# Performance work log

Measured on AMD Instinct MI355X. Metric: run time of the kernel, lower is better.

## Reference

```python
import jax, jax.numpy as jnp
import numpy as np

B, D, H, L, E, NL, P, IMG, NT = 32, 768, 8, 6, 8, 256, 16, 224, 10
G = IMG // P          # 14 patches per side
NP = G * G            # 196 patches
HD = D // H           # 96 head dim
TOPK = 2
KEEP = 0.25
EPS = 1e-5


def layer_norm(x, g, b):
    m = x.mean(-1, keepdims=True)
    v = ((x - m) ** 2).mean(-1, keepdims=True)
    return (x - m) / jnp.sqrt(v + EPS) * g + b


def mha(q, kv, in_w, in_b, out_w, out_b):
    # torch nn.MultiheadAttention: packed in_proj (3D, D), out_proj (D, D)
    wq, wk, wv = in_w[:D], in_w[D:2 * D], in_w[2 * D:]
    bq, bk, bv = in_b[:D], in_b[D:2 * D], in_b[2 * D:]

    def heads(x, w, b):
        y = x @ w.T + b                               # (B, S, D)
        return y.reshape(x.shape[0], x.shape[1], H, HD).transpose(0, 2, 1, 3)

    Q = heads(q, wq, bq)
    K = heads(kv, wk, bk)
    V = heads(kv, wv, bv)
    scores = jnp.einsum('bhqd,bhkd->bhqk', Q, K) / np.sqrt(HD).astype(np.float32)
    attn = jax.nn.softmax(scores, axis=-1)
    o = jnp.einsum('bhqk,bhkd->bhqd', attn, V)
    o = o.transpose(0, 2, 1, 3).reshape(q.shape[0], q.shape[1], D)
    return o @ out_w.T + out_b


def moe(x, rw, rb, w1, b1, w2, b2):
    # top-2 routing; renormalize the top-k weights with a second softmax
    Bq, S, _ = x.shape
    T = Bq * S
    xt = x.reshape(T, D)
    probs = jax.nn.softmax(xt @ rw.T + rb, axis=-1)       # (T, E)
    tw, ti = jax.lax.top_k(probs, TOPK)                   # (T, K)
    tw = jax.nn.softmax(tw, axis=-1)
    # combine weights per expert: (T, E), >0 only for the chosen experts
    combine = (jax.nn.one_hot(ti, E, dtype=x.dtype) * tw[..., None]).sum(axis=1)
    out = jnp.zeros_like(xt)
    for e in range(E):  # fixed small expert count
        h = jax.nn.gelu(xt @ w1[e].T + b1[e], approximate=False)
        out = out + (h @ w2[e].T + b2[e]) * combine[:, e:e + 1]
    return out.reshape(Bq, S, D)


def _forward(images, type_ids, mask_noise, conv_w, conv_b, pos_emb, type_emb,
             latents, ca_in_w, ca_in_b, ca_out_w, ca_out_b, ca_ln_g, ca_ln_b,
             sa_in_w, sa_in_b, sa_out_w, sa_out_b, ln1_g, ln1_b,
             router_w, router_b, e_w1, e_b1, e_w2, e_b2, ln2_g, ln2_b):
    b = images.shape[0]
    # non-overlapping conv patch embed == unfold + matmul
    xp = images.reshape(b, 3, G, P, G, P).transpose(0, 2, 4, 1, 3, 5)
    xp = xp.reshape(b, NP, 3 * P * P)
    patches = xp @ conv_w.reshape(D, -1).T + conv_b        # (B, NP, D)
    patches = patches + pos_emb + type_emb[type_ids][:, None, :]
    # random masking: keep n_visible patches chosen by argsort of noise
    n_visible = int(NP * KEEP)
    order = jnp.argsort(mask_noise, axis=1)
    visible_indices = order[:, :n_visible]
    masked_indices = order[:, n_visible:]
    visible = jnp.take_along_axis(patches, visible_indices[:, :, None], axis=1)
    # cross attention from latents to visible patches
    lat = jnp.broadcast_to(latents, (b, NL, D))
    lat = layer_norm(lat + mha(lat, visible, ca_in_w, ca_in_b, ca_out_w, ca_out_b),
                     ca_ln_g, ca_ln_b)
    for l in range(L):
        a = mha(lat, lat, sa_in_w[l], sa_in_b[l], sa_out_w[l], sa_out_b[l])
        lat = layer_norm(lat + a, ln1_g[l], ln1_b[l])
        m = moe(lat, router_w[l], router_b[l], e_w1[l], e_b1[l], e_w2[l], e_b2[l])
        lat = layer_norm(lat + m, ln2_g[l], ln2_b[l])
    return lat, visible_indices, masked_indices


def setup_inputs() -> dict:
    key = jax.random.key(0)
    ks = jax.random.split(key, 16)
    r = lambda k, shape, s=0.02: jax.random.normal(k, shape, dtype=jnp.float32) * s
    z = lambda shape: jnp.zeros(shape, jnp.float32)
    o = lambda shape: jnp.ones(shape, jnp.float32)
    inp = {}
    inp['images'] = jax.random.normal(ks[0], (B, 3, IMG, IMG), dtype=jnp.float32)
    inp['type_ids'] = jax.random.randint(ks[1], (B,), 0, NT)
    inp['mask_noise'] = jax.random.uniform(ks[2], (B, NP), dtype=jnp.float32)
    inp['conv_w'] = r(ks[3], (D, 3, P, P))
    inp['conv_b'] = z((D,))
    inp['pos_emb'] = r(ks[4], (1, NP, D), 1.0)
    inp['type_emb'] = r(ks[5], (NT, D), 1.0)
    inp['latents'] = r(ks[6], (NL, D), 1.0)
    inp['ca_in_w'] = r(ks[7], (3 * D, D)); inp['ca_in_b'] = z((3 * D,))
    inp['ca_out_w'] = r(ks[8], (D, D)); inp['ca_out_b'] = z((D,))
    inp['ca_ln_g'] = o((D,)); inp['ca_ln_b'] = z((D,))
    inp['sa_in_w'] = r(ks[9], (L, 3 * D, D)); inp['sa_in_b'] = z((L, 3 * D))
    inp['sa_out_w'] = r(ks[10], (L, D, D)); inp['sa_out_b'] = z((L, D))
    inp['ln1_g'] = o((L, D)); inp['ln1_b'] = z((L, D))
    inp['router_w'] = r(ks[11], (L, E, D)); inp['router_b'] = z((L, E))
    inp['e_w1'] = r(ks[12], (L, E, 2 * D, D)); inp['e_b1'] = z((L, E, 2 * D))
    inp['e_w2'] = r(ks[13], (L, E, D, 2 * D)); inp['e_b2'] = z((L, E, D))
    inp['ln2_g'] = o((L, D)); inp['ln2_b'] = z((L, D))
    return inp


def reference(images, type_ids, mask_noise, conv_w, conv_b, pos_emb, type_emb,
              latents, ca_in_w, ca_in_b, ca_out_w, ca_out_b, ca_ln_g, ca_ln_b,
              sa_in_w, sa_in_b, sa_out_w, sa_out_b, ln1_g, ln1_b,
              router_w, router_b, e_w1, e_b1, e_w2, e_b2, ln2_g, ln2_b):
    return _forward(images, type_ids, mask_noise, conv_w, conv_b, pos_emb,
                    type_emb, latents, ca_in_w, ca_in_b, ca_out_w, ca_out_b,
                    ca_ln_g, ca_ln_b, sa_in_w, sa_in_b, sa_out_w, sa_out_b,
                    ln1_g, ln1_b, router_w, router_b, e_w1, e_b1, e_w2, e_b2,
                    ln2_g, ln2_b)
```

## Files before the change

kernel.cpp:

```cpp
#include <hip/hip_runtime.h>

typedef unsigned short u16;
typedef unsigned int u32;
typedef __attribute__((ext_vector_type(8))) u16 u16x8;
typedef __attribute__((ext_vector_type(8))) __bf16 bf16x8;
typedef __attribute__((ext_vector_type(4))) float f32x4;

#define DEV static __device__ __forceinline__

DEV float b2f(u16 u){ unsigned int i = ((unsigned int)u)<<16; float f; __builtin_memcpy(&f,&i,4); return f; }
DEV u16 f2b(float f){ unsigned int x; __builtin_memcpy(&x,&f,4); x = x + 0x7fffu + ((x>>16)&1u); return (u16)(x>>16); }

DEV void gll16(const u16* g, u16* l){
    __builtin_amdgcn_global_load_lds(
        (const __attribute__((address_space(1))) u32*)(const void*)g,
        (__attribute__((address_space(3))) u32*)(void*)l, 16, 0, 0);
}

template<bool F32>
DEV u16x8 ld8(const void* base, long off){
    if constexpr (F32){
        const float* p = (const float*)base + off;
        float4 a = *(const float4*)p;
        float4 b = *(const float4*)(p+4);
        u16x8 r;
        r[0]=f2b(a.x); r[1]=f2b(a.y); r[2]=f2b(a.z); r[3]=f2b(a.w);
        r[4]=f2b(b.x); r[5]=f2b(b.y); r[6]=f2b(b.z); r[7]=f2b(b.w);
        return r;
    } else {
        return *(const u16x8*)((const u16*)base + off);
    }
}
template<bool F32>
DEV const void* vadd(const void* p, long elems){
    if constexpr (F32) return (const void*)((const float*)p + elems);
    else               return (const void*)((const u16*)p + elems);
}

#define LAT_ELEMS 6291456
#define NVIS 49
#define NMASK 147
#define T_TOK 8192
#define MOE_CAP 17408
#define MOE_HALF 8704
#define KOFF 6291456L
#define VOFF 12582912L

__global__ __launch_bounds__(256) void wconv(const float* __restrict__ src, u16* __restrict__ dst, long n)
{
    long i = ((long)blockIdx.x*256 + threadIdx.x)*8;
    if (i >= n) return;
    *(u16x8*)(dst + i) = ld8<true>(src, i);
}

__global__ __launch_bounds__(256) void argsort_k(const float* __restrict__ noise,
                                                 int* __restrict__ order,
                                                 float* __restrict__ dout,
                                                 u16* __restrict__ zbuf)
{
    __shared__ float vals[196];
    __shared__ int ord[196];
    int b = blockIdx.x, tid = threadIdx.x;
    if (b == 0 && tid < 128) zbuf[tid] = 0;
    if (tid < 196) vals[tid] = noise[b*196 + tid];
    __syncthreads();
    if (tid < 196){
        float vi = vals[tid]; int rank = 0;
        for (int j=0;j<196;j++){ float vj = vals[j]; rank += (vj < vi) || (vj == vi && j < tid); }
        ord[rank] = tid;
    }
    __syncthreads();
    if (tid < 196){
        int v = ord[tid];
        order[b*196 + tid] = v;
        if (tid < NVIS) dout[LAT_ELEMS + b*NVIS + tid] = (float)v;
        else            dout[LAT_ELEMS + 32*NVIS + b*NMASK + (tid - NVIS)] = (float)v;
    }
}

__global__ __launch_bounds__(256) void patch_gather(const float* __restrict__ images,
                                                    const int* __restrict__ order,
                                                    u16* __restrict__ Ap)
{
    int i = blockIdx.x*256 + threadIdx.x;
    int t = i/48, kc = i - t*48;
    if (t >= 1664) return;
    if (t >= 1568){
        u16x8 z{};
        *(u16x8*)(Ap + (long)t*768 + kc*16)     = z;
        *(u16x8*)(Ap + (long)t*768 + kc*16 + 8) = z;
        return;
    }
    int b = t/49, vi = t - b*49;
    int p = order[b*196 + vi];
    int c = kc >> 4, py = kc & 15;
    int gy = p/14, gx = p - gy*14;
    const float* src = images + (((long)(b*3 + c)*224 + gy*16 + py)*224 + gx*16);
    u16x8 o0 = ld8<true>(src, 0);
    u16x8 o1 = ld8<true>(src, 8);
    *(u16x8*)(Ap + (long)t*768 + kc*16)     = o0;
    *(u16x8*)(Ap + (long)t*768 + kc*16 + 8) = o1;
}

__global__ __launch_bounds__(256) void add_pos_type(u16* __restrict__ vis,
                                                    const int* __restrict__ order,
                                                    const int* __restrict__ type_ids,
                                                    const float* __restrict__ pos,
                                                    const float* __restrict__ temb)
{
    int i = blockIdx.x*256 + threadIdx.x;
    int t = i/96, dc = (i - t*96)*8;
    if (t >= 1568) return;
    int b = t/49, vi = t - b*49;
    int p = order[b*196 + vi], tb = type_ids[b];
    u16x8 a = *(u16x8*)(vis + (long)t*768 + dc);
    const float* pp = pos  + (long)p*768 + dc;
    const float* tt = temb + (long)tb*768 + dc;
    float4 p0 = *(const float4*)pp, p1 = *(const float4*)(pp+4);
    float4 t0 = *(const float4*)tt, t1 = *(const float4*)(tt+4);
    u16x8 o;
    o[0]=f2b(b2f(a[0])+p0.x+t0.x); o[1]=f2b(b2f(a[1])+p0.y+t0.y);
    o[2]=f2b(b2f(a[2])+p0.z+t0.z); o[3]=f2b(b2f(a[3])+p0.w+t0.w);
    o[4]=f2b(b2f(a[4])+p1.x+t1.x); o[5]=f2b(b2f(a[5])+p1.y+t1.y);
    o[6]=f2b(b2f(a[6])+p1.z+t1.z); o[7]=f2b(b2f(a[7])+p1.w+t1.w);
    *(u16x8*)(vis + (long)t*768 + dc) = o;
}

template<int BK, int MT, bool BIAS, bool GELU, int GRP, bool AF32, bool BF32, bool SWZ, bool GLL>
__global__ __launch_bounds__(256,4) void gemm_nt(
    const void* __restrict__ A, const void* __restrict__ B, const float* __restrict__ bias,
    u16* __restrict__ C,
    int M, int N, int K, int lda, int ldb, int ldc,
    float scale, int ZLO, int NB,
    long sAh, long sAl, long sBh, long sBl, long sCh, long sCl,
    const int* __restrict__ aoff, const int* __restrict__ tos, const u16* __restrict__ zbuf,
    int row_base, long sBE, long sBiasE)
{
    int bx = blockIdx.x, by = blockIdx.y;
    if (SWZ){
        int nx = gridDim.x, ny = gridDim.y;
        int nwg = nx*ny;
        int flat = by*nx + bx;
        int q = nwg >> 3, r = nwg & 7;
        int xcd = flat & 7, idx = flat >> 3;
        int wg = (xcd < r ? xcd*(q+1) : r*(q+1) + (xcd - r)*q) + idx;
        bx = wg % nx; by = wg / nx;
    }
    int z = blockIdx.z; int zh = z / ZLO, zl = z - zh*ZLO;
    const void* Ab = vadd<AF32>(A, zh*sAh + zl*sAl);
    const void* Bb = vadd<BF32>(B, zh*sBh + zl*sBl);
    u16* Cb = C + zh*sCh + zl*sCl;
    const float* biasb = bias;
    int row0 = by*MT, col0 = bx*128;
    int lim = 0;
    if (GRP == 1 || GRP == 2){
        lim = aoff[8];
        int g0 = row_base + row0;
        if (g0 >= lim) return;
        int e = 0;
        #pragma unroll
        for (int i=1;i<8;i++) if (g0 >= aoff[i]) e = i;
        Bb = vadd<BF32>(B, (long)e*sBE);
        if (BIAS) biasb = bias + (long)e*sBiasE;
    }
    constexpr int SP = GLL ? BK : BK + 8;
    constexpr int MR = MT/32;
    __shared__ __align__(16) u16 As[MT*SP];
    __shared__ __align__(16) u16 Bs[128*SP];
    int tid = threadIdx.x;
    int lane = tid & 63, wv = tid >> 6;
    int wr = (wv>>1)*(MT/2), wc = (wv&1)*64;
    f32x4 acc[MR][4];
    #pragma unroll
    for (int m=0;m<MR;m++){
        #pragma unroll
        for (int n=0;n<4;n++) acc[m][n] = f32x4{0.f,0.f,0.f,0.f};
    }
    constexpr int RPC = BK/8;
    constexpr int RPI = 64/RPC;
    constexpr int NJA = MT*RPC/256;
    constexpr int NJB = 128*RPC/256;
    constexpr int PER = 128*RPC/256;
    int tA[4];
    if (GRP == 1){
        #pragma unroll
        for (int j=0;j<NJA;j++){
            int r = wv*(MT/4) + j*RPI + (lane/RPC);
            tA[j] = tos[row_base + row0 + r];
        }
    }
    for (int k0=0; k0<K; k0+=BK){
        if constexpr (GLL){
            int ch = lane % RPC;
            #pragma unroll
            for (int j=0;j<NJA;j++){
                int r  = wv*(MT/4) + j*RPI + (lane/RPC);
                const u16* sa;
                if (GRP == 1){
                    int t = tA[j];
                    sa = (t >= 0) ? (const u16*)Ab + (long)t*lda + k0 + ch*8 : zbuf + ch*8;
                } else {
                    sa = (const u16*)Ab + (long)(row0+r)*lda + k0 + ch*8;
                }
                gll16(sa, As + (wv*(MT/4) + j*RPI)*BK);
            }
            #pragma unroll
            for (int j=0;j<NJB;j++){
                int r = wv*32 + j*RPI + (lane/RPC);
                const u16* sb = (col0 + r < NB) ? (const u16*)Bb + (long)(col0+r)*ldb + k0 + ch*8
                                                : zbuf + ch*8;
                gll16(sb, Bs + (wv*32 + j*RPI)*BK);
            }
        } else if constexpr (MT == 128){
            #pragma unroll
            for (int j=0;j<PER;j++){
                int c = j*256 + tid;
                int r = c / RPC, cc = (c - r*RPC)*8;
                u16x8 va{}, vb{};
                if (GRP == 1){
                    int t = tA[j];
                    if (t >= 0) va = ld8<AF32>(Ab, (long)t*lda + k0 + cc);
                } else {
                    va = ld8<AF32>(Ab, (long)(row0+r)*lda + k0 + cc);
                }
                if (col0 + r < NB) vb = ld8<BF32>(Bb, (long)(col0+r)*ldb + k0 + cc);
                *(u16x8*)(As + r*SP + cc) = va;
                *(u16x8*)(Bs + r*SP + cc) = vb;
            }
        }
        __syncthreads();
        #pragma unroll
        for (int kk=0; kk<BK/32; kk++){
            bf16x8 af[MR], bg[4];
            #pragma unroll
            for (int m=0;m<MR;m++)
                af[m] = *(const bf16x8*)(As + (wr + m*16 + (lane&15))*SP + kk*32 + (lane>>4)*8);
            #pragma unroll
            for (int n=0;n<4;n++)
                bg[n] = *(const bf16x8*)(Bs + (wc + n*16 + (lane&15))*SP + kk*32 + (lane>>4)*8);
            #pragma unroll
            for (int m=0;m<MR;m++){
                #pragma unroll
                for (int n=0;n<4;n++)
                    acc[m][n] = __builtin_amdgcn_mfma_f32_16x16x32_bf16(af[m], bg[n], acc[m][n], 0,0,0);
            }
        }
        __syncthreads();
    }
    if (GRP == 3){
        #pragma unroll
        for (int m=0;m<MR;m++){
            int rbase = row0 + wr + m*16 + ((lane>>4)<<2);
            #pragma unroll
            for (int n=0;n<4;n++){
                int col = col0 + wc + n*16 + (lane&15);
                float bv = biasb[col];
                if (col < 1536){
                    u16* base = (col < 768) ? Cb : Cb + sBE - 768;
                    #pragma unroll
                    for (int j=0;j<4;j++)
                        base[(long)(rbase+j)*768 + col] = f2b(acc[m][n][j]*scale + bv);
                } else {
                    int c96 = col - 1536;
                    int h = c96/96, d = c96 - h*96;
                    ushort4 o4;
                    o4.x = f2b(acc[m][n][0]*scale + bv);
                    o4.y = f2b(acc[m][n][1]*scale + bv);
                    o4.z = f2b(acc[m][n][2]*scale + bv);
                    o4.w = f2b(acc[m][n][3]*scale + bv);
                    *(ushort4*)(Cb + sBiasE + ((long)((rbase>>8)*8 + h)*96 + d)*256 + (rbase & 255)) = o4;
                }
            }
        }
        return;
    }
    #pragma unroll
    for (int m=0;m<MR;m++){
        int rbase = row0 + wr + m*16 + ((lane>>4)<<2);
        #pragma unroll
        for (int n=0;n<4;n++){
            int col = col0 + wc + n*16 + (lane&15);
            if (col < N){
                float bv = BIAS ? biasb[col] : 0.f;
                #pragma unroll
                for (int j=0;j<4;j++){
                    int row = rbase + j;
                    bool ok = (row < M);
                    if (GRP == 1 || GRP == 2) ok = ok && (row_base + row) < lim;
                    if (ok){
                        float v = acc[m][n][j]*scale + bv;
                        if (GELU) v = 0.5f*v*(1.f + erff(v*0.70710678118f));
                        u16 ov = f2b(v);
                        if (GRP == 2){
                            Cb[(long)(row_base + row)*ldc + col] = ov;
                        } else {
                            Cb[(long)row*ldc + col] = ov;
                        }
                    }
                }
            }
        }
    }
}

__global__ __launch_bounds__(256,4) void scores_sm(const u16* __restrict__ Q,
                                                   const u16* __restrict__ K,
                                                   u16* __restrict__ S)
{
    __shared__ __align__(16) u16 As[64*32];
    __shared__ __align__(16) u16 Bs[256*32];
    int z = blockIdx.y;
    int b = z >> 3, h = z & 7;
    const u16* Ab = Q + (long)b*196608 + h*96 + (long)blockIdx.x*64*768;
    const u16* Bb = K + (long)b*196608 + h*96;
    int tid = threadIdx.x, lane = tid & 63, wv = tid >> 6;
    f32x4 acc[16];
    #pragma unroll
    for (int n=0;n<16;n++) acc[n] = f32x4{0.f,0.f,0.f,0.f};
    int ch = lane & 3, rr = lane >> 2;
    for (int k0=0;k0<96;k0+=32){
        gll16(Ab + (long)(wv*16 + rr)*768 + k0 + ch*8, As + (wv*16)*32);
        #pragma unroll
        for (int jj=0;jj<4;jj++)
            gll16(Bb + (long)(wv*64 + jj*16 + rr)*768 + k0 + ch*8, Bs + (wv*64 + jj*16)*32);
        __syncthreads();
        bf16x8 af = *(const bf16x8*)(As + (wv*16 + (lane&15))*32 + (lane>>4)*8);
        #pragma unroll
        for (int n=0;n<16;n++){
            bf16x8 bg = *(const bf16x8*)(Bs + (n*16 + (lane&15))*32 + (lane>>4)*8);
            acc[n] = __builtin_amdgcn_mfma_f32_16x16x32_bf16(af, bg, acc[n], 0,0,0);
        }
        __syncthreads();
    }
    const float SCL = 0.10206207f;
    u16* Sz = S + (long)z*65536 + (long)blockIdx.x*64*256;
    #pragma unroll
    for (int j=0;j<4;j++){
        float mx = -1e30f;
        #pragma unroll
        for (int n=0;n<16;n++) mx = fmaxf(mx, acc[n][j]);
        #pragma unroll
        for (int off=8; off>=1; off>>=1) mx = fmaxf(mx, __shfl_xor(mx, off, 64));
        float ev[16]; float sum = 0.f;
        #pragma unroll
        for (int n=0;n<16;n++){ ev[n] = __expf((acc[n][j]-mx)*SCL); sum += ev[n]; }
        #pragma unroll
        for (int off=8; off>=1; off>>=1) sum += __shfl_xor(sum, off, 64);
        float inv = 1.f/sum;
        int row = wv*16 + ((lane>>4)<<2) + j;
        #pragma unroll
        for (int n=0;n<16;n++) Sz[(long)row*256 + n*16 + (lane&15)] = f2b(ev[n]*inv);
    }
}

__global__ __launch_bounds__(256) void ca_attn(const u16* __restrict__ Qc,
                                               const u16* __restrict__ KV,
                                               u16* __restrict__ attn_out)
{
    __shared__ float Sm[256*49];
    __shared__ u16 KVs[49*96];
    int b = blockIdx.x, h = blockIdx.y, q = threadIdx.x;
    for (int i=q; i<49*96; i+=256){ int k=i/96, d=i-k*96; KVs[i] = KV[(long)(b*49+k)*1536 + h*96 + d]; }
    __syncthreads();
    float qv[96];
    #pragma unroll
    for (int d=0;d<96;d++) qv[d] = b2f(Qc[(long)q*768 + h*96 + d]);
    for (int k=0;k<49;k++){
        float a = 0.f;
        #pragma unroll
        for (int d=0;d<96;d++) a += qv[d]*b2f(KVs[k*96+d]);
        Sm[q*49+k] = a*0.10206207f;
    }
    __syncthreads();
    for (int i=q; i<49*96; i+=256){ int k=i/96, d=i-k*96; KVs[i] = KV[(long)(b*49+k)*1536 + 768 + h*96 + d]; }
    float mx = -1e30f;
    for (int k=0;k<49;k++) mx = fmaxf(mx, Sm[q*49+k]);
    float sum = 0.f;
    for (int k=0;k<49;k++){ float e = __expf(Sm[q*49+k]-mx); Sm[q*49+k]=e; sum+=e; }
    float inv = 1.f/sum;
    __syncthreads();
    for (int d=0;d<96;d++){
        float a = 0.f;
        for (int k=0;k<49;k++) a += Sm[q*49+k]*b2f(KVs[k*96+d]);
        attn_out[(long)(b*256+q)*768 + h*96 + d] = f2b(a*inv);
    }
}

template<int MODE, bool ROUTE>
__global__ __launch_bounds__(256) void ln_k(
    const float* __restrict__ res, int resmod,
    const u16* __restrict__ add,
    const u16* __restrict__ OutE, const int* __restrict__ sot, const float2* __restrict__ w01,
    const float* __restrict__ g, const float* __restrict__ bb,
    const float* __restrict__ rw, const float* __restrict__ rb,
    int2* __restrict__ e01o, float2* __restrict__ w01o,
    float* __restrict__ out, u16* __restrict__ outb, int T)
{
    int wid = threadIdx.x >> 6, lane = threadIdx.x & 63;
    int t = blockIdx.x*4 + wid; if (t >= T) return;
    const float* rp = res + (long)(t % resmod)*768;
    float x[12];
    #pragma unroll
    for (int j=0;j<3;j++){
        float4 v = *(const float4*)(rp + j*256 + lane*4);
        x[j*4+0]=v.x; x[j*4+1]=v.y; x[j*4+2]=v.z; x[j*4+3]=v.w;
    }
    if (MODE == 0){
        const u16* ap = add + (long)t*768;
        #pragma unroll
        for (int j=0;j<3;j++){
            ushort4 v = *(const ushort4*)(ap + j*256 + lane*4);
            x[j*4+0]+=b2f(v.x); x[j*4+1]+=b2f(v.y); x[j*4+2]+=b2f(v.z); x[j*4+3]+=b2f(v.w);
        }
    } else {
        int s0 = sot[2*t], s1 = sot[2*t+1];
        float2 w = w01[t];
        const u16* p0 = OutE + (long)s0*768;
        const u16* p1 = OutE + (long)s1*768;
        #pragma unroll
        for (int j=0;j<3;j++){
            ushort4 v0 = *(const ushort4*)(p0 + j*256 + lane*4);
            ushort4 v1 = *(const ushort4*)(p1 + j*256 + lane*4);
            x[j*4+0] += w.x*b2f(v0.x) + w.y*b2f(v1.x);
            x[j*4+1] += w.x*b2f(v0.y) + w.y*b2f(v1.y);
            x[j*4+2] += w.x*b2f(v0.z) + w.y*b2f(v1.z);
            x[j*4+3] += w.x*b2f(v0.w) + w.y*b2f(v1.w);
        }
    }
    float s = 0.f;
    #pragma unroll
    for (int i=0;i<12;i++) s += x[i];
    #pragma unroll
    for (int off=32; off>=1; off>>=1) s += __shfl_xor(s, off, 64);
    float m = s*(1.f/768.f);
    float s2 = 0.f;
    #pragma unroll
    for (int i=0;i<12;i++){ float d = x[i]-m; s2 += d*d; }
    #pragma unroll
    for (int off=32; off>=1; off>>=1) s2 += __shfl_xor(s2, off, 64);
    float rstd = rsqrtf(s2*(1.f/768.f) + 1e-5f);
    float y[12];
    #pragma unroll
    for (int j=0;j<3;j++){
        int col = j*256 + lane*4;
        float4 gg = *(const float4*)(g + col);
        float4 bv = *(const float4*)(bb + col);
        y[j*4+0] = (x[j*4+0]-m)*rstd*gg.x + bv.x;
        y[j*4+1] = (x[j*4+1]-m)*rstd*gg.y + bv.y;
        y[j*4+2] = (x[j*4+2]-m)*rstd*gg.z + bv.z;
        y[j*4+3] = (x[j*4+3]-m)*rstd*gg.w + bv.w;
        float4 o; o.x=y[j*4+0]; o.y=y[j*4+1]; o.z=y[j*4+2]; o.w=y[j*4+3];
        *(float4*)(out + (long)t*768 + col) = o;
        if (outb != nullptr){
            ushort4 ob;
            ob.x = f2b(o.x); ob.y = f2b(o.y); ob.z = f2b(o.z); ob.w = f2b(o.w);
            *(ushort4*)(outb + (long)t*768 + col) = ob;
        }
    }
    if (ROUTE){
        float part[8];
        #pragma unroll
        for (int e=0;e<8;e++){
            const float* wp = rw + e*768;
            float a = 0.f;
            #pragma unroll
            for (int j=0;j<3;j++){
                float4 w4 = *(const float4*)(wp + j*256 + lane*4);
                a += y[j*4+0]*w4.x + y[j*4+1]*w4.y + y[j*4+2]*w4.z + y[j*4+3]*w4.w;
            }
            part[e] = a;
        }
        #pragma unroll
        for (int e=0;e<8;e++){
            #pragma unroll
            for (int off=32; off>=1; off>>=1) part[e] += __shfl_xor(part[e], off, 64);
        }
        if (lane == 0){
            float pe[8];
            float mx = -1e30f;
            #pragma unroll
            for (int e=0;e<8;e++){ pe[e] = part[e] + rb[e]; mx = fmaxf(mx, pe[e]); }
            float sum = 0.f;
            #pragma unroll
            for (int e=0;e<8;e++){ pe[e] = __expf(pe[e]-mx); sum += pe[e]; }
            float inv = 1.f/sum;
            #pragma unroll
            for (int e=0;e<8;e++) pe[e] *= inv;
            int i0 = 0;
            #pragma unroll
            for (int e=1;e<8;e++) if (pe[e] > pe[i0]) i0 = e;
            int i1 = -1;
            for (int e=0;e<8;e++){ if (e == i0) continue; if (i1 < 0 || pe[e] > pe[i1]) i1 = e; }
            float ex = __expf(pe[i1] - pe[i0]);
            float w0 = 1.f/(1.f+ex), w1 = ex/(1.f+ex);
            e01o[t] = int2{i0, i1};
            w01o[t] = float2{w0, w1};
        }
    }
}

__global__ __launch_bounds__(1024) void route_build(const int2* __restrict__ e01,
                                                    int* __restrict__ aoff_g,
                                                    int* __restrict__ tos, int* __restrict__ sot,
                                                    u16* __restrict__ zbuf)
{
    __shared__ int wsum[8][16];
    __shared__ int wbase[8][16];
    __shared__ int aoff_s[9];
    int tid = threadIdx.x, lane = tid & 63, wid = tid >> 6;
    for (int s = tid; s < MOE_CAP; s += 1024) tos[s] = -1;
    if (tid < 128) zbuf[tid] = 0;
    int t0 = tid * 8;
    int lc[8];
    #pragma unroll
    for (int e=0;e<8;e++) lc[e] = 0;
    #pragma unroll
    for (int i=0;i<8;i++){
        int2 e = e01[t0+i];
        lc[e.x]++; lc[e.y]++;
    }
    int excl[8];
    #pragma unroll
    for (int e=0;e<8;e++){
        int sc = lc[e];
        #pragma unroll
        for (int off=1; off<64; off<<=1){
            int n = __shfl_up(sc, off, 64);
            if (lane >= off) sc += n;
        }
        excl[e] = sc - lc[e];
        if (lane == 63) wsum[e][wid] = sc;
    }
    __syncthreads();
    if (tid == 0){
        int tot = 0;
        #pragma unroll
        for (int e=0;e<8;e++){
            int s = 0;
            #pragma unroll
            for (int w=0;w<16;w++){ wbase[e][w] = s; s += wsum[e][w]; }
            aoff_s[e] = tot;
            tot += (s + 127) & ~127;
        }
        aoff_s[8] = tot;
        #pragma unroll
        for (int e=0;e<9;e++) aoff_g[e] = aoff_s[e];
    }
    __syncthreads();
    int cur[8];
    #pragma unroll
    for (int e=0;e<8;e++) cur[e] = aoff_s[e] + wbase[e][wid] + excl[e];
    #pragma unroll
    for (int i=0;i<8;i++){
        int t = t0 + i;
        int2 e = e01[t];
        int s0 = cur[e.x]++;
        tos[s0] = t; sot[2*t]   = s0;
        int s1 = cur[e.y]++;
        tos[s1] = t; sot[2*t+1] = s1;
    }
}

extern "C" void kernel_launch(void* const* d_in, const int* in_sizes, int n_in,
                              void* d_out, int out_size, void* d_ws, size_t ws_size,
                              hipStream_t stream)
{
    (void)in_sizes; (void)n_in; (void)out_size;
    const float* images   = (const float*)d_in[0];
    const int*   type_ids = (const int*)d_in[1];
    const float* noise    = (const float*)d_in[2];
    const float* conv_w   = (const float*)d_in[3];
    const float* conv_b   = (const float*)d_in[4];
    const float* pos_emb  = (const float*)d_in[5];
    const float* type_emb = (const float*)d_in[6];
    const float* latents  = (const float*)d_in[7];
    const float* ca_in_w  = (const float*)d_in[8];
    const float* ca_in_b  = (const float*)d_in[9];
    const float* ca_out_w = (const float*)d_in[10];
    const float* ca_out_b = (const float*)d_in[11];
    const float* ca_ln_g  = (const float*)d_in[12];
    const float* ca_ln_b  = (const float*)d_in[13];
    const float* sa_in_w  = (const float*)d_in[14];
    const float* sa_in_b  = (const float*)d_in[15];
    const float* sa_out_w = (const float*)d_in[16];
    const float* sa_out_b = (const float*)d_in[17];
    const float* ln1_g    = (const float*)d_in[18];
    const float* ln1_b    = (const float*)d_in[19];
    const float* router_w = (const float*)d_in[20];
    const float* router_b = (const float*)d_in[21];
    const float* e_w1     = (const float*)d_in[22];
    const float* e_b1     = (const float*)d_in[23];
    const float* e_w2     = (const float*)d_in[24];
    const float* e_b2     = (const float*)d_in[25];
    const float* ln2_g    = (const float*)d_in[26];
    const float* ln2_b    = (const float*)d_in[27];
    float* dout = (float*)d_out;
    float* lat  = dout;

    char* p = (char*)d_ws;
    auto alloc = [&](size_t n)->char*{ char* r = p; p += (n + 255) & ~(size_t)255; return r; };
    int*    order  = (int*)   alloc(32*196*4);
    int2*   e01    = (int2*)  alloc((size_t)T_TOK*8);
    float2* w01    = (float2*)alloc((size_t)T_TOK*8);
    int*    aoff   = (int*)   alloc(64);
    int*    tos    = (int*)   alloc((size_t)MOE_CAP*4);
    int*    sot    = (int*)   alloc((size_t)T_TOK*2*4);
    u16*    zbuf   = (u16*)   alloc(256);
    size_t aux_used = (size_t)(p - (char*)d_ws);
    const size_t WB_BYTES = 92798976ull + 260702208ull;
    bool wb  = ws_size >= aux_used + WB_BYTES;
    bool big = wb || ws_size >= aux_used + 92798976ull;
    u16* ar = (u16*)alloc(wb ? WB_BYTES : (big ? 92798976ull : 71303168ull));
    u16* latb   = big ? ar : nullptr;
    u16* common = big ? ar + 6291456 : ar;
    u16* wbufA  = wb ? ar + 6291456 + 40108032 : nullptr;
    u16* Ap  = common;
    u16* vis = common + 1277952;
    u16* KV  = common + 2555904;
    u16* Qc  = common + 5111808;
    u16* caO = common + 5308416;
    u16* caM = common + 11599872;
    u16* Qb  = common;
    u16* Vt  = common + VOFF;
    u16* S   = common + 18874368;
    u16* aO  = common;
    u16* mha = common + KOFF;
    u16* Hbuf = common;
    u16* OutE = common + (big ? 26738688 : 13369344);
    u16* cwb      = wbufA;
    u16* cainb    = wbufA + 589824;
    u16* caoutb   = wbufA + 2359296;
    u16* winbAll  = wbufA + 2949120;
    u16* woutbAll = wbufA + 13565952;
    u16* w1bAll   = wbufA + 17104896;
    u16* w2bAll   = wbufA + 73728000;

    const float ONE = 1.0f;
    const long Z0 = 0;

    argsort_k<<<32, 256, 0, stream>>>(noise, order, dout, zbuf);
    patch_gather<<<312, 256, 0, stream>>>(images, order, Ap);
    if (wb){
        wconv<<<288, 256, 0, stream>>>(conv_w, cwb, 589824);
        wconv<<<864, 256, 0, stream>>>(ca_in_w, cainb, 1769472);
        wconv<<<288, 256, 0, stream>>>(ca_out_w, caoutb, 589824);
        wconv<<<5184, 256, 0, stream>>>(sa_in_w, winbAll, 10616832);
        wconv<<<1728, 256, 0, stream>>>(sa_out_w, woutbAll, 3538944);
        wconv<<<27648, 256, 0, stream>>>(e_w1, w1bAll, 56623104);
        wconv<<<27648, 256, 0, stream>>>(e_w2, w2bAll, 56623104);
        gemm_nt<64,64,true,false,0,false,false,true,true><<<dim3(6,26,1),256,0,stream>>>(Ap, cwb, conv_b, vis,
            1664,768,768, 768,768,768, ONE, 1, 768, Z0,Z0,Z0,Z0,Z0,Z0, nullptr,nullptr,zbuf,0, Z0,Z0);
        add_pos_type<<<588, 256, 0, stream>>>(vis, order, type_ids, pos_emb, type_emb);
        gemm_nt<64,128,true,false,0,true,false,true,false><<<dim3(6,2,1),256,0,stream>>>(latents, cainb, ca_in_b, Qc,
            256,768,768, 768,768,768, ONE, 1, 768, Z0,Z0,Z0,Z0,Z0,Z0, nullptr,nullptr,zbuf,0, Z0,Z0);
        gemm_nt<64,64,true,false,0,false,false,true,true><<<dim3(12,26,1),256,0,stream>>>(vis, cainb + 589824, ca_in_b + 768, KV,
            1664,1536,768, 768,768,1536, ONE, 1, 1536, Z0,Z0,Z0,Z0,Z0,Z0, nullptr,nullptr,zbuf,0, Z0,Z0);
        ca_attn<<<dim3(32,8), 256, 0, stream>>>(Qc, KV, caO);
        gemm_nt<64,64,true,false,0,false,false,true,true><<<dim3(6,128,1),256,0,stream>>>(caO, caoutb, ca_out_b, caM,
            T_TOK,768,768, 768,768,768, ONE, 1, 768, Z0,Z0,Z0,Z0,Z0,Z0, nullptr,nullptr,zbuf,0, Z0,Z0);
    } else {
        gemm_nt<64,128,true,false,0,false,true,false,false><<<dim3(6,13,1),256,0,stream>>>(Ap, conv_w, conv_b, vis,
            1664,768,768, 768,768,768, ONE, 1, 768, Z0,Z0,Z0,Z0,Z0,Z0, nullptr,nullptr,zbuf,0, Z0,Z0);
        add_pos_type<<<588, 256, 0, stream>>>(vis, order, type_ids, pos_emb, type_emb);
        gemm_nt<64,128,true,false,0,true,true,false,false><<<dim3(6,2,1),256,0,stream>>>(latents, ca_in_w, ca_in_b, Qc,
            256,768,768, 768,768,768, ONE, 1, 768, Z0,Z0,Z0,Z0,Z0,Z0, nullptr,nullptr,zbuf,0, Z0,Z0);
        gemm_nt<64,128,true,false,0,false,true,false,false><<<dim3(12,13,1),256,0,stream>>>(vis, ca_in_w + 768*768, ca_in_b + 768, KV,
            1664,1536,768, 768,768,1536, ONE, 1, 1536, Z0,Z0,Z0,Z0,Z0,Z0, nullptr,nullptr,zbuf,0, Z0,Z0);
        ca_attn<<<dim3(32,8), 256, 0, stream>>>(Qc, KV, caO);
        gemm_nt<64,128,true,false,0,false,true,false,false><<<dim3(6,64,1),256,0,stream>>>(caO, ca_out_w, ca_out_b, caM,
            T_TOK,768,768, 768,768,768, ONE, 1, 768, Z0,Z0,Z0,Z0,Z0,Z0, nullptr,nullptr,zbuf,0, Z0,Z0);
    }
    ln_k<0,false><<<2048, 256, 0, stream>>>(latents, 256, caM, nullptr,nullptr,nullptr, ca_ln_g, ca_ln_b,
        nullptr,nullptr,nullptr,nullptr, lat, latb, T_TOK);

    for (int l=0; l<6; l++){
        const float* b_in  = sa_in_b  + l*2304;
        const float* b_out = sa_out_b + l*768;
        const float* b1 = e_b1 + l*8*1536;
        const float* b2 = e_b2 + l*8*768;
        const float* rwl = router_w + l*8*768;
        const float* rbl = router_b + l*8;
        if (wb){
            const u16* winb  = winbAll  + (long)l*1769472;
            const u16* woutb = woutbAll + (long)l*589824;
            const u16* w1b   = w1bAll   + (long)l*9437184;
            const u16* w2b   = w2bAll   + (long)l*9437184;
            gemm_nt<64,128,true,false,3,false,false,true,true><<<dim3(18,64,1),256,0,stream>>>(latb, winb, b_in, Qb,
                T_TOK,2304,768, 768,768,0, ONE, 1, 2304, Z0,Z0,Z0,Z0,Z0,Z0, nullptr,nullptr,zbuf,0, KOFF, VOFF);
            scores_sm<<<dim3(4,256), 256, 0, stream>>>(Qb, Qb + KOFF, S);
            gemm_nt<64,64,false,false,0,false,false,false,true><<<dim3(1,4,256),256,0,stream>>>(S, Vt, nullptr, aO,
                256,96,256, 256,256,768, ONE, 8, 96, 524288,65536, 196608,24576, 196608,96, nullptr,nullptr,zbuf,0, Z0,Z0);
            gemm_nt<64,64,true,false,0,false,false,true,true><<<dim3(6,128,1),256,0,stream>>>(aO, woutb, b_out, mha,
                T_TOK,768,768, 768,768,768, ONE, 1, 768, Z0,Z0,Z0,Z0,Z0,Z0, nullptr,nullptr,zbuf,0, Z0,Z0);
            ln_k<0,true><<<2048, 256, 0, stream>>>(lat, T_TOK, mha, nullptr,nullptr,nullptr, ln1_g + l*768, ln1_b + l*768,
                rwl, rbl, e01, w01, lat, latb, T_TOK);
            route_build<<<1, 1024, 0, stream>>>(e01, aoff, tos, sot, zbuf);
            gemm_nt<64,128,true,true,1,false,false,true,true><<<dim3(12,136,1),256,0,stream>>>(latb, w1b, b1, Hbuf,
                MOE_CAP,1536,768, 768,768,1536, ONE, 1, 1536, Z0,Z0,Z0,Z0,Z0,Z0,
                aoff, tos, zbuf, 0, (long)1536*768, 1536);
            gemm_nt<64,128,true,false,2,false,false,true,true><<<dim3(6,136,1),256,0,stream>>>(Hbuf, w2b, b2, OutE,
                MOE_CAP,768,1536, 1536,1536,768, ONE, 1, 768, Z0,Z0,Z0,Z0,Z0,Z0,
                aoff, tos, zbuf, 0, (long)768*1536, 768);
            ln_k<1,false><<<2048, 256, 0, stream>>>(lat, T_TOK, nullptr, OutE, sot, w01, ln2_g + l*768, ln2_b + l*768,
                nullptr,nullptr,nullptr,nullptr, lat, latb, T_TOK);
        } else {
            const float* w_in  = sa_in_w  + (long)l*2304*768;
            const float* w_out = sa_out_w + (long)l*768*768;
            const float* w1 = e_w1 + (long)l*8*1536*768;
            const float* w2 = e_w2 + (long)l*8*768*1536;
            if (big){
                gemm_nt<64,128,true,false,3,false,true,false,false><<<dim3(18,64,1),256,0,stream>>>(latb, w_in, b_in, Qb,
                    T_TOK,2304,768, 768,768,0, ONE, 1, 2304, Z0,Z0,Z0,Z0,Z0,Z0, nullptr,nullptr,zbuf,0, KOFF, VOFF);
            } else {
                gemm_nt<64,128,true,false,3,true,true,false,false><<<dim3(18,64,1),256,0,stream>>>(lat, w_in, b_in, Qb,
                    T_TOK,2304,768, 768,768,0, ONE, 1, 2304, Z0,Z0,Z0,Z0,Z0,Z0, nullptr,nullptr,zbuf,0, KOFF, VOFF);
            }
            scores_sm<<<dim3(4,256), 256, 0, stream>>>(Qb, Qb + KOFF, S);
            gemm_nt<64,128,false,false,0,false,false,false,false><<<dim3(1,2,256),256,0,stream>>>(S, Vt, nullptr, aO,
                256,96,256, 256,256,768, ONE, 8, 96, 524288,65536, 196608,24576, 196608,96, nullptr,nullptr,zbuf,0, Z0,Z0);
            gemm_nt<64,128,true,false,0,false,true,false,false><<<dim3(6,64,1),256,0,stream>>>(aO, w_out, b_out, mha,
                T_TOK,768,768, 768,768,768, ONE, 1, 768, Z0,Z0,Z0,Z0,Z0,Z0, nullptr,nullptr,zbuf,0, Z0,Z0);
            ln_k<0,true><<<2048, 256, 0, stream>>>(lat, T_TOK, mha, nullptr,nullptr,nullptr, ln1_g + l*768, ln1_b + l*768,
                rwl, rbl, e01, w01, lat, latb, T_TOK);
            route_build<<<1, 1024, 0, stream>>>(e01, aoff, tos, sot, zbuf);
            if (big){
                gemm_nt<64,128,true,true,1,false,true,false,false><<<dim3(12,136,1),256,0,stream>>>(latb, w1, b1, Hbuf,
                    MOE_CAP,1536,768, 768,768,1536, ONE, 1, 1536, Z0,Z0,Z0,Z0,Z0,Z0,
                    aoff, tos, zbuf, 0, (long)1536*768, 1536);
                gemm_nt<64,128,true,false,2,false,true,false,false><<<dim3(6,136,1),256,0,stream>>>(Hbuf, w2, b2, OutE,
                    MOE_CAP,768,1536, 1536,1536,768, ONE, 1, 768, Z0,Z0,Z0,Z0,Z0,Z0,
                    aoff, tos, zbuf, 0, (long)768*1536, 768);
            } else {
                for (int rb2=0; rb2<MOE_CAP; rb2+=MOE_HALF){
                    gemm_nt<64,128,true,true,1,true,true,false,false><<<dim3(12,68,1),256,0,stream>>>(lat, w1, b1, Hbuf,
                        MOE_HALF,1536,768, 768,768,1536, ONE, 1, 1536, Z0,Z0,Z0,Z0,Z0,Z0,
                        aoff, tos, zbuf, rb2, (long)1536*768, 1536);
                    gemm_nt<64,128,true,false,2,false,true,false,false><<<dim3(6,68,1),256,0,stream>>>(Hbuf, w2, b2, OutE,
                        MOE_HALF,768,1536, 1536,1536,768, ONE, 1, 768, Z0,Z0,Z0,Z0,Z0,Z0,
                        aoff, tos, zbuf, rb2, (long)768*1536, 768);
                }
            }
            ln_k<1,false><<<2048, 256, 0, stream>>>(lat, T_TOK, nullptr, OutE, sot, w01, ln2_g + l*768, ln2_b + l*768,
                nullptr,nullptr,nullptr,nullptr, lat, latb, T_TOK);
        }
    }
}
```

Measured before the change: 2.220 ms.

## Double-buffer LDS in GEMM with async global_load_lds prefetch pipeline

Adds a PIPE template flag to the bf16 GEMM that uses two LDS buffers. While MFMAs run on the current K-tile, the next tile is prefetched with global_load_lds, using vmcnt waits and raw s_barriers in place of the load-sync-compute-sync loop. It is enabled for the QKV projection and both MoE expert GEMMs on the bf16 path, aiming to hide global load latency behind compute. LDS use doubles, which may reduce occupancy with four blocks per CU requested.

```diff
diff --git a/kernel.cpp b/kernel.cpp
--- a/kernel.cpp
+++ b/kernel.cpp
@@ -126,7 +126,7 @@
     *(u16x8*)(vis + (long)t*768 + dc) = o;
 }
 
-template<int BK, int MT, bool BIAS, bool GELU, int GRP, bool AF32, bool BF32, bool SWZ, bool GLL>
+template<int BK, int MT, bool BIAS, bool GELU, int GRP, bool AF32, bool BF32, bool SWZ, bool GLL, bool PIPE>
 __global__ __launch_bounds__(256,4) void gemm_nt(
     const void* __restrict__ A, const void* __restrict__ B, const float* __restrict__ bias,
     u16* __restrict__ C,
@@ -165,8 +165,9 @@
     }
     constexpr int SP = GLL ? BK : BK + 8;
     constexpr int MR = MT/32;
-    __shared__ __align__(16) u16 As[MT*SP];
-    __shared__ __align__(16) u16 Bs[128*SP];
+    constexpr int NBUF = PIPE ? 2 : 1;
+    __shared__ __align__(16) u16 As[NBUF*MT*SP];
+    __shared__ __align__(16) u16 Bs[NBUF*128*SP];
     int tid = threadIdx.x;
     int lane = tid & 63, wv = tid >> 6;
     int wr = (wv>>1)*(MT/2), wc = (wv&1)*64;
@@ -180,6 +181,7 @@
     constexpr int RPI = 64/RPC;
     constexpr int NJA = MT*RPC/256;
     constexpr int NJB = 128*RPC/256;
+    constexpr int NISSUE = NJA + NJB;
     constexpr int PER = 128*RPC/256;
     int tA[4];
     if (GRP == 1){
@@ -189,55 +191,38 @@
             tA[j] = tos[row_base + row0 + r];
         }
     }
-    for (int k0=0; k0<K; k0+=BK){
-        if constexpr (GLL){
-            int ch = lane % RPC;
-            #pragma unroll
-            for (int j=0;j<NJA;j++){
-                int r  = wv*(MT/4) + j*RPI + (lane/RPC);
-                const u16* sa;
-                if (GRP == 1){
-                    int t = tA[j];
-                    sa = (t >= 0) ? (const u16*)Ab + (long)t*lda + k0 + ch*8 : zbuf + ch*8;
-                } else {
-                    sa = (const u16*)Ab + (long)(row0+r)*lda + k0 + ch*8;
-                }
-                gll16(sa, As + (wv*(MT/4) + j*RPI)*BK);
-            }
-            #pragma unroll
-            for (int j=0;j<NJB;j++){
-                int r = wv*32 + j*RPI + (lane/RPC);
-                const u16* sb = (col0 + r < NB) ? (const u16*)Bb + (long)(col0+r)*ldb + k0 + ch*8
-                                                : zbuf + ch*8;
-                gll16(sb, Bs + (wv*32 + j*RPI)*BK);
-            }
-        } else if constexpr (MT == 128){
-            #pragma unroll
-            for (int j=0;j<PER;j++){
-                int c = j*256 + tid;
-                int r = c / RPC, cc = (c - r*RPC)*8;
-                u16x8 va{}, vb{};
-                if (GRP == 1){
-                    int t = tA[j];
-                    if (t >= 0) va = ld8<AF32>(Ab, (long)t*lda + k0 + cc);
-                } else {
-                    va = ld8<AF32>(Ab, (long)(row0+r)*lda + k0 + cc);
-                }
-                if (col0 + r < NB) vb = ld8<BF32>(Bb, (long)(col0+r)*ldb + k0 + cc);
-                *(u16x8*)(As + r*SP + cc) = va;
-                *(u16x8*)(Bs + r*SP + cc) = vb;
-            }
-        }
-        __syncthreads();
+    auto stage = [&](int k0, int boff){
+        int ch = lane % RPC;
+        #pragma unroll
+        for (int j=0;j<NJA;j++){
+            int r  = wv*(MT/4) + j*RPI + (lane/RPC);
+            const u16* sa;
+            if (GRP == 1){
+                int t = tA[j];
+                sa = (t >= 0) ? (const u16*)Ab + (long)t*lda + k0 + ch*8 : zbuf + ch*8;
+            } else {
+                sa = (const u16*)Ab + (long)(row0+r)*lda + k0 + ch*8;
+            }
+            gll16(sa, As + boff*MT*SP + (wv*(MT/4) + j*RPI)*BK);
+        }
+        #pragma unroll
+        for (int j=0;j<NJB;j++){
+            int r = wv*32 + j*RPI + (lane/RPC);
+            const u16* sb = (col0 + r < NB) ? (const u16*)Bb + (long)(col0+r)*ldb + k0 + ch*8
+                                            : zbuf + ch*8;
+            gll16(sb, Bs + boff*128*SP + (wv*32 + j*RPI)*BK);
+        }
+    };
+    auto mfma_tile = [&](int boff){
         #pragma unroll
         for (int kk=0; kk<BK/32; kk++){
             bf16x8 af[MR], bg[4];
             #pragma unroll
             for (int m=0;m<MR;m++)
-                af[m] = *(const bf16x8*)(As + (wr + m*16 + (lane&15))*SP + kk*32 + (lane>>4)*8);
+                af[m] = *(const bf16x8*)(As + boff*MT*SP + (wr + m*16 + (lane&15))*SP + kk*32 + (lane>>4)*8);
             #pragma unroll
             for (int n=0;n<4;n++)
-                bg[n] = *(const bf16x8*)(Bs + (wc + n*16 + (lane&15))*SP + kk*32 + (lane>>4)*8);
+                bg[n] = *(const bf16x8*)(Bs + boff*128*SP + (wc + n*16 + (lane&15))*SP + kk*32 + (lane>>4)*8);
             #pragma unroll
             for (int m=0;m<MR;m++){
                 #pragma unroll
@@ -245,7 +230,50 @@
                     acc[m][n] = __builtin_amdgcn_mfma_f32_16x16x32_bf16(af[m], bg[n], acc[m][n], 0,0,0);
             }
         }
-        __syncthreads();
+    };
+    if constexpr (PIPE && GLL){
+        int NT = K/BK;
+        stage(0, 0);
+        for (int t=0; t<NT; ++t){
+            int cur = t & 1;
+            if (t+1 < NT){
+                stage((t+1)*BK, cur^1);
+                asm volatile("s_waitcnt vmcnt(%0)" :: "n"(NISSUE) : "memory");
+            } else {
+                asm volatile("s_waitcnt vmcnt(0)" ::: "memory");
+            }
+            __builtin_amdgcn_sched_barrier(0);
+            __builtin_amdgcn_s_barrier();
+            __builtin_amdgcn_sched_barrier(0);
+            mfma_tile(cur);
+            __builtin_amdgcn_sched_barrier(0);
+            __builtin_amdgcn_s_barrier();
+        }
+    } else {
+        for (int k0=0; k0<K; k0+=BK){
+            if constexpr (GLL){
+                stage(k0, 0);
+            } else if constexpr (MT == 128){
+                #pragma unroll
+                for (int j=0;j<PER;j++){
+                    int c = j*256 + tid;
+                    int r = c / RPC, cc = (c - r*RPC)*8;
+                    u16x8 va{}, vb{};
+                    if (GRP == 1){
+                        int t = tA[j];
+                        if (t >= 0) va = ld8<AF32>(Ab, (long)t*lda + k0 + cc);
+                    } else {
+                        va = ld8<AF32>(Ab, (long)(row0+r)*lda + k0 + cc);
+                    }
+                    if (col0 + r < NB) vb = ld8<BF32>(Bb, (long)(col0+r)*ldb + k0 + cc);
+                    *(u16x8*)(As + r*SP + cc) = va;
+                    *(u16x8*)(Bs + r*SP + cc) = vb;
+                }
+            }
+            __syncthreads();
+            mfma_tile(0);
+            __syncthreads();
+        }
     }
     if (GRP == 3){
         #pragma unroll
@@ -648,26 +676,26 @@
         wconv<<<1728, 256, 0, stream>>>(sa_out_w, woutbAll, 3538944);
         wconv<<<27648, 256, 0, stream>>>(e_w1, w1bAll, 56623104);
         wconv<<<27648, 256, 0, stream>>>(e_w2, w2bAll, 56623104);
-        gemm_nt<64,64,true,false,0,false,false,true,true><<<dim3(6,26,1),256,0,stream>>>(Ap, cwb, conv_b, vis,
+        gemm_nt<64,64,true,false,0,false,false,true,true,false><<<dim3(6,26,1),256,0,stream>>>(Ap, cwb, conv_b, vis,
             1664,768,768, 768,768,768, ONE, 1, 768, Z0,Z0,Z0,Z0,Z0,Z0, nullptr,nullptr,zbuf,0, Z0,Z0);
         add_pos_type<<<588, 256, 0, stream>>>(vis, order, type_ids, pos_emb, type_emb);
-        gemm_nt<64,128,true,false,0,true,false,true,false><<<dim3(6,2,1),256,0,stream>>>(latents, cainb, ca_in_b, Qc,
+        gemm_nt<64,128,true,false,0,true,false,true,false,false><<<dim3(6,2,1),256,0,stream>>>(latents, cainb, ca_in_b, Qc,
             256,768,768, 768,768,768, ONE, 1, 768, Z0,Z0,Z0,Z0,Z0,Z0, nullptr,nullptr,zbuf,0, Z0,Z0);
-        gemm_nt<64,64,true,false,0,false,false,true,true><<<dim3(12,26,1),256,0,stream>>>(vis, cainb + 589824, ca_in_b + 768, KV,
+        gemm_nt<64,64,true,false,0,false,false,true,true,false><<<dim3(12,26,1),256,0,stream>>>(vis, cainb + 589824, ca_in_b + 768, KV,
             1664,1536,768, 768,768,1536, ONE, 1, 1536, Z0,Z0,Z0,Z0,Z0,Z0, nullptr,nullptr,zbuf,0, Z0,Z0);
         ca_attn<<<dim3(32,8), 256, 0, stream>>>(Qc, KV, caO);
-        gemm_nt<64,64,true,false,0,false,false,true,true><<<dim3(6,128,1),256,0,stream>>>(caO, caoutb, ca_out_b, caM,
+        gemm_nt<64,64,true,false,0,false,false,true,true,false><<<dim3(6,128,1),256,0,stream>>>(caO, caoutb, ca_out_b, caM,
             T_TOK,768,768, 768,768,768, ONE, 1, 768, Z0,Z0,Z0,Z0,Z0,Z0, nullptr,nullptr,zbuf,0, Z0,Z0);
     } else {
-        gemm_nt<64,128,true,false,0,false,true,false,false><<<dim3(6,13,1),256,0,stream>>>(Ap, conv_w, conv_b, vis,
+        gemm_nt<64,128,true,false,0,false,true,false,false,false><<<dim3(6,13,1),256,0,stream>>>(Ap, conv_w, conv_b, vis,
             1664,768,768, 768,768,768, ONE, 1, 768, Z0,Z0,Z0,Z0,Z0,Z0, nullptr,nullptr,zbuf,0, Z0,Z0);
         add_pos_type<<<588, 256, 0, stream>>>(vis, order, type_ids, pos_emb, type_emb);
-        gemm_nt<64,128,true,false,0,true,true,false,false><<<dim3(6,2,1),256,0,stream>>>(latents, ca_in_w, ca_in_b, Qc,
+        gemm_nt<64,128,true,false,0,true,true,false,false,false><<<dim3(6,2,1),256,0,stream>>>(latents, ca_in_w, ca_in_b, Qc,
             256,768,768, 768,768,768, ONE, 1, 768, Z0,Z0,Z0,Z0,Z0,Z0, nullptr,nullptr,zbuf,0, Z0,Z0);
-        gemm_nt<64,128,true,false,0,false,true,false,false><<<dim3(12,13,1),256,0,stream>>>(vis, ca_in_w + 768*768, ca_in_b + 768, KV,
+        gemm_nt<64,128,true,false,0,false,true,false,false,false><<<dim3(12,13,1),256,0,stream>>>(vis, ca_in_w + 768*768, ca_in_b + 768, KV,
             1664,1536,768, 768,768,1536, ONE, 1, 1536, Z0,Z0,Z0,Z0,Z0,Z0, nullptr,nullptr,zbuf,0, Z0,Z0);
         ca_attn<<<dim3(32,8), 256, 0, stream>>>(Qc, KV, caO);
-        gemm_nt<64,128,true,false,0,false,true,false,false><<<dim3(6,64,1),256,0,stream>>>(caO, ca_out_w, ca_out_b, caM,
+        gemm_nt<64,128,true,false,0,false,true,false,false,false><<<dim3(6,64,1),256,0,stream>>>(caO, ca_out_w, ca_out_b, caM,
             T_TOK,768,768, 768,768,768, ONE, 1, 768, Z0,Z0,Z0,Z0,Z0,Z0, nullptr,nullptr,zbuf,0, Z0,Z0);
     }
     ln_k<0,false><<<2048, 256, 0, stream>>>(latents, 256, caM, nullptr,nullptr,nullptr, ca_ln_g, ca_ln_b,
@@ -685,20 +713,20 @@
             const u16* woutb = woutbAll + (long)l*589824;
             const u16* w1b   = w1bAll   + (long)l*9437184;
             const u16* w2b   = w2bAll   + (long)l*9437184;
-            gemm_nt<64,128,true,false,3,false,false,true,true><<<dim3(18,64,1),256,0,stream>>>(latb, winb, b_in, Qb,
+            gemm_nt<64,128,true,false,3,false,false,true,true,true><<<dim3(18,64,1),256,0,stream>>>(latb, winb, b_in, Qb,
                 T_TOK,2304,768, 768,768,0, ONE, 1, 2304, Z0,Z0,Z0,Z0,Z0,Z0, nullptr,nullptr,zbuf,0, KOFF, VOFF);
             scores_sm<<<dim3(4,256), 256, 0, stream>>>(Qb, Qb + KOFF, S);
-            gemm_nt<64,64,false,false,0,false,false,false,true><<<dim3(1,4,256),256,0,stream>>>(S, Vt, nullptr, aO,
+            gemm_nt<64,64,false,false,0,false,false,false,true,false><<<dim3(1,4,256),256,0,stream>>>(S, Vt, nullptr, aO,
                 256,96,256, 256,256,768, ONE, 8, 96, 524288,65536, 196608,24576, 196608,96, nullptr,nullptr,zbuf,0, Z0,Z0);
-            gemm_nt<64,64,true,false,0,false,false,true,true><<<dim3(6,128,1),256,0,stream>>>(aO, woutb, b_out, mha,
+            gemm_nt<64,64,true,false,0,false,false,true,true,false><<<dim3(6,128,1),256,0,stream>>>(aO, woutb, b_out, mha,
                 T_TOK,768,768, 768,768,768, ONE, 1, 768, Z0,Z0,Z0,Z0,Z0,Z0, nullptr,nullptr,zbuf,0, Z0,Z0);
             ln_k<0,true><<<2048, 256, 0, stream>>>(lat, T_TOK, mha, nullptr,nullptr,nullptr, ln1_g + l*768, ln1_b + l*768,
                 rwl, rbl, e01, w01, lat, latb, T_TOK);
             route_build<<<1, 1024, 0, stream>>>(e01, aoff, tos, sot, zbuf);
-            gemm_nt<64,128,true,true,1,false,false,true,true><<<dim3(12,136,1),256,0,stream>>>(latb, w1b, b1, Hbuf,
+            gemm_nt<64,128,true,true,1,false,false,true,true,true><<<dim3(12,136,1),256,0,stream>>>(latb, w1b, b1, Hbuf,
                 MOE_CAP,1536,768, 768,768,1536, ONE, 1, 1536, Z0,Z0,Z0,Z0,Z0,Z0,
                 aoff, tos, zbuf, 0, (long)1536*768, 1536);
-            gemm_nt<64,128,true,false,2,false,false,true,true><<<dim3(6,136,1),256,0,stream>>>(Hbuf, w2b, b2, OutE,
+            gemm_nt<64,128,true,false,2,false,false,true,true,true><<<dim3(6,136,1),256,0,stream>>>(Hbuf, w2b, b2, OutE,
                 MOE_CAP,768,1536, 1536,1536,768, ONE, 1, 768, Z0,Z0,Z0,Z0,Z0,Z0,
                 aoff, tos, zbuf, 0, (long)768*1536, 768);
             ln_k<1,false><<<2048, 256, 0, stream>>>(lat, T_TOK, nullptr, OutE, sot, w01, ln2_g + l*768, ln2_b + l*768,
@@ -709,33 +737,33 @@
             const float* w1 = e_w1 + (long)l*8*1536*768;
             const float* w2 = e_w2 + (long)l*8*768*1536;
             if (big){
-                gemm_nt<64,128,true,false,3,false,true,false,false><<<dim3(18,64,1),256,0,stream>>>(latb, w_in, b_in, Qb,
+                gemm_nt<64,128,true,false,3,false,true,false,false,false><<<dim3(18,64,1),256,0,stream>>>(latb, w_in, b_in, Qb,
                     T_TOK,2304,768, 768,768,0, ONE, 1, 2304, Z0,Z0,Z0,Z0,Z0,Z0, nullptr,nullptr,zbuf,0, KOFF, VOFF);
             } else {
-                gemm_nt<64,128,true,false,3,true,true,false,false><<<dim3(18,64,1),256,0,stream>>>(lat, w_in, b_in, Qb,
+                gemm_nt<64,128,true,false,3,true,true,false,false,false><<<dim3(18,64,1),256,0,stream>>>(lat, w_in, b_in, Qb,
                     T_TOK,2304,768, 768,768,0, ONE, 1, 2304, Z0,Z0,Z0,Z0,Z0,Z0, nullptr,nullptr,zbuf,0, KOFF, VOFF);
             }
             scores_sm<<<dim3(4,256), 256, 0, stream>>>(Qb, Qb + KOFF, S);
-            gemm_nt<64,128,false,false,0,false,false,false,false><<<dim3(1,2,256),256,0,stream>>>(S, Vt, nullptr, aO,
+            gemm_nt<64,128,false,false,0,false,false,false,false,false><<<dim3(1,2,256),256,0,stream>>>(S, Vt, nullptr, aO,
                 256,96,256, 256,256,768, ONE, 8, 96, 524288,65536, 196608,24576, 196608,96, nullptr,nullptr,zbuf,0, Z0,Z0);
-            gemm_nt<64,128,true,false,0,false,true,false,false><<<dim3(6,64,1),256,0,stream>>>(aO, w_out, b_out, mha,
+            gemm_nt<64,128,true,false,0,false,true,false,false,false><<<dim3(6,64,1),256,0,stream>>>(aO, w_out, b_out, mha,
                 T_TOK,768,768, 768,768,768, ONE, 1, 768, Z0,Z0,Z0,Z0,Z0,Z0, nullptr,nullptr,zbuf,0, Z0,Z0);
             ln_k<0,true><<<2048, 256, 0, stream>>>(lat, T_TOK, mha, nullptr,nullptr,nullptr, ln1_g + l*768, ln1_b + l*768,
                 rwl, rbl, e01, w01, lat, latb, T_TOK);
             route_build<<<1, 1024, 0, stream>>>(e01, aoff, tos, sot, zbuf);
             if (big){
-                gemm_nt<64,128,true,true,1,false,true,false,false><<<dim3(12,136,1),256,0,stream>>>(latb, w1, b1, Hbuf,
+                gemm_nt<64,128,true,true,1,false,true,false,false,false><<<dim3(12,136,1),256,0,stream>>>(latb, w1, b1, Hbuf,
                     MOE_CAP,1536,768, 768,768,1536, ONE, 1, 1536, Z0,Z0,Z0,Z0,Z0,Z0,
                     aoff, tos, zbuf, 0, (long)1536*768, 1536);
-                gemm_nt<64,128,true,false,2,false,true,false,false><<<dim3(6,136,1),256,0,stream>>>(Hbuf, w2, b2, OutE,
+                gemm_nt<64,128,true,false,2,false,true,false,false,false><<<dim3(6,136,1),256,0,stream>>>(Hbuf, w2, b2, OutE,
                     MOE_CAP,768,1536, 1536,1536,768, ONE, 1, 768, Z0,Z0,Z0,Z0,Z0,Z0,
                     aoff, tos, zbuf, 0, (long)768*1536, 768);
             } else {
                 for (int rb2=0; rb2<MOE_CAP; rb2+=MOE_HALF){
-                    gemm_nt<64,128,true,true,1,true,true,false,false><<<dim3(12,68,1),256,0,stream>>>(lat, w1, b1, Hbuf,
+                    gemm_nt<64,128,true,true,1,true,true,false,false,false><<<dim3(12,68,1),256,0,stream>>>(lat, w1, b1, Hbuf,
                         MOE_HALF,1536,768, 768,768,1536, ONE, 1, 1536, Z0,Z0,Z0,Z0,Z0,Z0,
                         aoff, tos, zbuf, rb2, (long)1536*768, 1536);
-                    gemm_nt<64,128,true,false,2,false,true,false,false><<<dim3(6,68,1),256,0,stream>>>(Hbuf, w2, b2, OutE,
+                    gemm_nt<64,128,true,false,2,false,true,false,false,false><<<dim3(6,68,1),256,0,stream>>>(Hbuf, w2, b2, OutE,
                         MOE_HALF,768,1536, 1536,1536,768, ONE, 1, 768, Z0,Z0,Z0,Z0,Z0,Z0,
                         aoff, tos, zbuf, rb2, (long)768*1536, 768);
                 }
```

New measurement: 2.777 ms. 25.1% more time.
